# Kernel optimization log

Measured on AMD Instinct MI355X. Metric: run time of the kernel, lower is better.

## Reference

```python
import jax, jax.numpy as jnp
import numpy as np

THRE = 0.5        # communication threshold
ALPHA = 0.8       # S_e / S_c mix in pattern gate
P_BIAS, P_WEIGHT = 0.1, 0.9
DILATE_K = 3
EPS = 1e-6


def warp_affine(src, M, out_hw):
    """torch F.affine_grid + F.grid_sample (bilinear, zeros padding, align_corners=False).
    src: (B,C,Hs,Ws), M: (B,2,3) normalized affine. Returns (B,C,Ho,Wo)."""
    B, C, Hs, Ws = src.shape
    Ho, Wo = out_hw
    xs = 2.0 * (jnp.arange(Wo, dtype=src.dtype) + 0.5) / Wo - 1.0
    ys = 2.0 * (jnp.arange(Ho, dtype=src.dtype) + 0.5) / Ho - 1.0
    gx, gy = jnp.meshgrid(xs, ys)                                   # (Ho,Wo)
    base = jnp.stack([gx, gy, jnp.ones_like(gx)], axis=-1)          # (Ho,Wo,3)
    g = jnp.einsum('bij,hwj->bhwi', M.astype(src.dtype), base)      # (B,Ho,Wo,2) x,y
    px = ((g[..., 0] + 1.0) * Ws - 1.0) * 0.5
    py = ((g[..., 1] + 1.0) * Hs - 1.0) * 0.5
    x0 = jnp.floor(px); y0 = jnp.floor(py)
    wx1 = px - x0; wx0 = 1.0 - wx1
    wy1 = py - y0; wy0 = 1.0 - wy1
    bidx = jnp.arange(B)[:, None, None]
    def samp(yi, xi):
        yi = yi.astype(jnp.int32); xi = xi.astype(jnp.int32)
        valid = (yi >= 0) & (yi < Hs) & (xi >= 0) & (xi < Ws)
        yc = jnp.clip(yi, 0, Hs - 1); xc = jnp.clip(xi, 0, Ws - 1)
        v = src[bidx, :, yc, xc]                                    # (B,Ho,Wo,C)
        return v * valid[..., None].astype(src.dtype)
    out = (samp(y0, x0) * (wy0 * wx0)[..., None]
         + samp(y0, x0 + 1) * (wy0 * wx1)[..., None]
         + samp(y0 + 1, x0) * (wy1 * wx0)[..., None]
         + samp(y0 + 1, x0 + 1) * (wy1 * wx1)[..., None])
    return jnp.transpose(out, (0, 3, 1, 2))


def masked_quantile(xf, mf, q):
    """torch.quantile(x[mask], q) with linear interpolation. xf:(N,HW) float, mf:(N,HW) bool."""
    xs = jnp.sort(jnp.where(mf, xf, jnp.inf), axis=-1)
    cnt = mf.sum(axis=-1)
    pos = q * jnp.maximum(cnt - 1, 0).astype(xf.dtype)
    lo = jnp.floor(pos).astype(jnp.int32)
    hi = jnp.ceil(pos).astype(jnp.int32)
    frac = pos - lo.astype(xf.dtype)
    vlo = jnp.take_along_axis(xs, lo[:, None], axis=-1)[:, 0]
    vhi = jnp.take_along_axis(xs, hi[:, None], axis=-1)[:, 0]
    val = vlo + frac * (vhi - vlo)
    return jnp.where(cnt > 0, val, jnp.zeros_like(val))


def qnorm01(x, mask, ql=0.2, qh=0.8):
    """_qnorm01_masked: per-image masked quantile normalization to [0,1]."""
    N = x.shape[0]
    xf = x.reshape(N, -1)
    mf = mask.reshape(N, -1) > 0
    lo = masked_quantile(xf, mf, ql)[:, None]
    hi = masked_quantile(xf, mf, qh)[:, None]
    y = jnp.clip((xf - lo) / (hi - lo + EPS), 0.0, 1.0) * mf.astype(x.dtype)
    return y.reshape(x.shape)


def pattern_gate(conf_b, feats_b, vis_b):
    """_build_pattern_gate. Returns P (1,1,H,W) on ego plane."""
    visf = (vis_b > 0).astype(feats_b.dtype)
    energy = jnp.mean(feats_b ** 2, axis=1, keepdims=True)          # (N,1,H,W)
    S_e = qnorm01(energy, vis_b) * visf
    S_c_raw = jnp.max(jax.nn.sigmoid(conf_b), axis=1, keepdims=True)  # A>1 branch
    S_c = qnorm01(S_c_raw, vis_b) * visf
    S_mix = ALPHA * S_e + (1.0 - ALPHA) * S_c
    D_e = qnorm01(1.0 - S_e[0:1], vis_b[0:1])
    D_c = qnorm01(1.0 - S_c[0:1], vis_b[0:1])
    D = (0.7 * D_e + 0.3 * D_c) * visf[0:1]
    m0 = vis_b[0:1].reshape(1, -1) > 0
    q20_e = masked_quantile(S_e[0:1].reshape(1, -1), m0, 0.2)[0]
    q20_c = masked_quantile(S_c[0:1].reshape(1, -1), m0, 0.2)[0]
    Ke = (S_e[0:1] <= q20_e) & (vis_b[0:1] > 0)
    Kc = (S_c[0:1] <= q20_c) & (vis_b[0:1] > 0)
    K_empty = (Ke & Kc).astype(feats_b.dtype)
    Sup_nei = jnp.mean(S_mix[1:] * visf[1:], axis=0, keepdims=True)
    P = D * Sup_nei * (1.0 - K_empty)
    return qnorm01(P, vis_b[0:1]) * visf[0:1]


def dilate(mask, k):
    if k <= 1:
        return mask
    return jax.lax.reduce_window(mask, -jnp.inf, jax.lax.max,
                                 (1, 1, k, k), (1, 1, 1, 1), 'SAME')


def owner_for_batch(feats_b, conf_b, vis_b, base_b):
    """_compute_owner_masks_from_comm for one batch group (N agents), eval mode
    (soft_tau=0 -> hard argmax owner), dual_ratio=0, dilate_k=3, supply='cls'."""
    N = feats_b.shape[0]
    visf = (vis_b > 0).astype(feats_b.dtype)
    S_full = jnp.clip(conf_b, 0.0, 1.0).mean(axis=1, keepdims=True) * visf
    P = pattern_gate(conf_b, feats_b, vis_b)                        # (1,1,H,W)
    S_b = S_full * (P_BIAS + P_WEIGHT * P)                          # broadcast over N
    scores = S_b * visf                                             # (N,1,H,W)
    winner = jnp.argmax(scores, axis=0)                             # (1,H,W)
    onehot = (jnp.arange(N)[:, None, None, None] == winner[None]).astype(feats_b.dtype)
    owner = onehot * (base_b > 0).astype(feats_b.dtype)
    return dilate(owner, DILATE_K)


def forward(x, psm_single, record_len, normalized_affine_matrix):
    B, L = normalized_affine_matrix.shape[:2]
    N = L  # uniform record_len assumed (record_len[b] == L for all b)
    sumN, C, H, W = x.shape
    A = psm_single.shape[1]
    # ego-view warp matrices t_matrix[0, :N] per batch, flattened to (B*N,2,3)
    M = normalized_affine_matrix[:, 0].reshape(B * N, 2, 3)
    ones = jnp.ones((B * N, 1, H, W), x.dtype)
    vis = warp_affine(ones, M, (H, W))          # warp masks
    conf = warp_affine(psm_single, M, (H, W))   # warped confidence maps
    wx = warp_affine(x, M, (H, W))              # warped features
    # Communication: where2comm-style threshold on max-sigmoid confidence; ego always ones
    comm_map = jnp.max(jax.nn.sigmoid(conf), axis=1, keepdims=True)
    comm = (comm_map > THRE).astype(x.dtype)
    comm = comm.reshape(B, N, 1, H, W).at[:, 0].set(1.0)            # (B,N,1,H,W)
    owner = jax.vmap(owner_for_batch)(
        wx.reshape(B, N, C, H, W), conf.reshape(B, N, A, H, W),
        vis.reshape(B, N, 1, H, W), comm)                           # (B,N,1,H,W)
    final = comm * owner
    wxm = wx.reshape(B, N, C, H, W) * final
    # effective rate over non-ego agents
    eff = final[:, 1:].sum(axis=(1, 2, 3, 4)) / ((N - 1) * H * W)
    effective_rate = eff.mean()
    x_out = wxm.max(axis=1)                                         # MaxFusion over agents
    return x_out, effective_rate


def setup_inputs():
    key = jax.random.key(0)
    k1, k2, k3 = jax.random.split(key, 3)
    B, N, C, A, H, W = 4, 5, 64, 2, 128, 256
    x = jax.random.normal(k1, (B * N, C, H, W), jnp.float32)
    psm_single = jax.random.normal(k2, (B * N, A, H, W), jnp.float32)
    record_len = jnp.full((B,), N, jnp.int32)
    eye = jnp.tile(jnp.array([[1.0, 0.0, 0.0], [0.0, 1.0, 0.0]], jnp.float32), (B, N, N, 1, 1))
    mats = eye + 0.05 * jax.random.normal(k3, (B, N, N, 2, 3), jnp.float32)
    return {"x": x, "psm_single": psm_single, "record_len": record_len,
            "normalized_affine_matrix": mats}


def reference(x, psm_single, record_len, normalized_affine_matrix):
    return forward(x, psm_single, record_len, normalized_affine_matrix)
```

## Files before the change

kernel.cpp:

```cpp
#include <hip/hip_runtime.h>

#define W_    256
#define H_    128
#define HW_   32768
#define NB    4
#define NA    5
#define NC    64
#define NIMG  20
#define EPS_  1e-6f

struct Taps { int o00,o01,o10,o11; float w00,w01,w10,w11; };

__device__ inline void proj_pt(float M0,float M1,float M2,float M3,float M4,float M5,
                               int h,int w,float&px,float&py){
  float gx = 2.0f*((float)w+0.5f)/(float)W_ - 1.0f;
  float gy = 2.0f*((float)h+0.5f)/(float)H_ - 1.0f;
  float X = M0*gx + M1*gy + M2;
  float Y = M3*gx + M4*gy + M5;
  px = ((X+1.0f)*(float)W_ - 1.0f)*0.5f;
  py = ((Y+1.0f)*(float)H_ - 1.0f)*0.5f;
}

__device__ inline Taps make_taps(const float* __restrict__ M, int h, int w){
  float px,py; proj_pt(M[0],M[1],M[2],M[3],M[4],M[5],h,w,px,py);
  float x0f=floorf(px), y0f=floorf(py);
  float wx1=px-x0f, wx0=1.f-wx1, wy1=py-y0f, wy0=1.f-wy1;
  int x0=(int)x0f, y0=(int)y0f, x1=x0+1, y1=y0+1;
  bool vx0=(x0>=0)&&(x0<W_), vx1=(x1>=0)&&(x1<W_);
  bool vy0=(y0>=0)&&(y0<H_), vy1=(y1>=0)&&(y1<H_);
  int cx0=min(max(x0,0),W_-1), cx1=min(max(x1,0),W_-1);
  int cy0=min(max(y0,0),H_-1), cy1=min(max(y1,0),H_-1);
  Taps t;
  t.o00=cy0*W_+cx0; t.o01=cy0*W_+cx1; t.o10=cy1*W_+cx0; t.o11=cy1*W_+cx1;
  t.w00=(vy0&&vx0)?(wy0*wx0):0.f;
  t.w01=(vy0&&vx1)?(wy0*wx1):0.f;
  t.w10=(vy1&&vx0)?(wy1*wx0):0.f;
  t.w11=(vy1&&vx1)?(wy1*wx1):0.f;
  return t;
}

__device__ inline float clip01(float v){ return fminf(fmaxf(v,0.f),1.f); }
__device__ inline float sigmoidf_(float v){
  if (v>=0.f){ float e=expf(-v); return 1.f/(1.f+e); }
  float e=expf(v); return e/(1.f+e);
}
__device__ inline float quantv(int cnt, float q, float vlo, float vhi){
  if (cnt<=0) return 0.f;
  float pos = q*(float)(cnt-1);
  float frac = pos - floorf(pos);
  return vlo + frac*(vhi-vlo);
}
__device__ inline float ge_f(float t, float lo, float hi){
  return clip01((t-lo)/(hi-lo+EPS_));
}

#define SBAR __builtin_amdgcn_sched_barrier(0)

__global__ void k_init(int* counters){ if (threadIdx.x==0) counters[0] = 0; }

__global__ __launch_bounds__(64) void k_gram(
  const float* __restrict__ x, float* __restrict__ gram)
{
  int lane = threadIdx.x;
  int bx = blockIdx.x;
  int bn = bx >> 7;
  int r  = bx & 127;
  int rn = min(r+1, H_-1);
  int col = lane<<2;
  const float* xb = x + (size_t)bn*NC*HW_;
  float4 aA={0,0,0,0}, aBx={0,0,0,0}, aBy={0,0,0,0}, aBd1={0,0,0,0}, aBd2={0,0,0,0};
  #pragma unroll 4
  for (int c=0;c<NC;++c){
    const float* pc = xb + (size_t)c*HW_;
    float4 a = *reinterpret_cast<const float4*>(pc + r*W_  + col);
    float4 b = *reinterpret_cast<const float4*>(pc + rn*W_ + col);
    float axn = __shfl(a.x, lane+1, 64);
    float bxn = __shfl(b.x, lane+1, 64);
    aA.x  = fmaf(a.x,a.x,aA.x);  aA.y  = fmaf(a.y,a.y,aA.y);
    aA.z  = fmaf(a.z,a.z,aA.z);  aA.w  = fmaf(a.w,a.w,aA.w);
    aBx.x = fmaf(a.x,a.y,aBx.x); aBx.y = fmaf(a.y,a.z,aBx.y);
    aBx.z = fmaf(a.z,a.w,aBx.z); aBx.w = fmaf(a.w,axn,aBx.w);
    aBy.x = fmaf(a.x,b.x,aBy.x); aBy.y = fmaf(a.y,b.y,aBy.y);
    aBy.z = fmaf(a.z,b.z,aBy.z); aBy.w = fmaf(a.w,b.w,aBy.w);
    aBd1.x= fmaf(a.x,b.y,aBd1.x);aBd1.y= fmaf(a.y,b.z,aBd1.y);
    aBd1.z= fmaf(a.z,b.w,aBd1.z);aBd1.w= fmaf(a.w,bxn,aBd1.w);
    aBd2.x= fmaf(a.y,b.x,aBd2.x);aBd2.y= fmaf(a.z,b.y,aBd2.y);
    aBd2.z= fmaf(a.w,b.z,aBd2.z);aBd2.w= fmaf(axn,b.w,aBd2.w);
  }
  float* g0 = gram + (((size_t)bn*HW_ + (size_t)r*W_ + col)<<3);
  float4 lo,hi;
  lo.x=aA.x; lo.y=aBx.x; lo.z=aBy.x; lo.w=aBd1.x; hi.x=aBd2.x; hi.y=0; hi.z=0; hi.w=0;
  *reinterpret_cast<float4*>(g0+ 0)=lo; *reinterpret_cast<float4*>(g0+ 4)=hi;
  lo.x=aA.y; lo.y=aBx.y; lo.z=aBy.y; lo.w=aBd1.y; hi.x=aBd2.y;
  *reinterpret_cast<float4*>(g0+ 8)=lo; *reinterpret_cast<float4*>(g0+12)=hi;
  lo.x=aA.z; lo.y=aBx.z; lo.z=aBy.z; lo.w=aBd1.z; hi.x=aBd2.z;
  *reinterpret_cast<float4*>(g0+16)=lo; *reinterpret_cast<float4*>(g0+20)=hi;
  lo.x=aA.w; lo.y=aBx.w; lo.z=aBy.w; lo.w=aBd1.w; hi.x=aBd2.w;
  *reinterpret_cast<float4*>(g0+24)=lo; *reinterpret_cast<float4*>(g0+28)=hi;
}

__global__ __launch_bounds__(256) void k_warp2(
  const float* __restrict__ psm, const float* __restrict__ nam,
  const float* __restrict__ gram,
  float* __restrict__ vis, float* __restrict__ scraw, float* __restrict__ sfull,
  float* __restrict__ energy)
{
  int w = threadIdx.x, h = blockIdx.x, bn = blockIdx.y;
  int b = bn/NA, n = bn - b*NA;
  const float* M = nam + (size_t)(b*NA*NA + n)*6;
  float px,py; proj_pt(M[0],M[1],M[2],M[3],M[4],M[5],h,w,px,py);
  float x0f=floorf(px), y0f=floorf(py);
  float wx1=px-x0f, wx0=1.f-wx1, wy1=py-y0f, wy0=1.f-wy1;
  int x0=(int)x0f, y0=(int)y0f, x1=x0+1, y1=y0+1;
  bool vx0=(x0>=0)&&(x0<W_), vx1=(x1>=0)&&(x1<W_);
  bool vy0=(y0>=0)&&(y0<H_), vy1=(y1>=0)&&(y1<H_);
  int cx0=min(max(x0,0),W_-1), cx1=min(max(x1,0),W_-1);
  int cy0=min(max(y0,0),H_-1), cy1=min(max(y1,0),H_-1);
  float w00=(vy0&&vx0)?(wy0*wx0):0.f;
  float w01=(vy0&&vx1)?(wy0*wx1):0.f;
  float w10=(vy1&&vx0)?(wy1*wx0):0.f;
  float w11=(vy1&&vx1)?(wy1*wx1):0.f;
  int i00=cy0*W_+cx0, i01=cy0*W_+cx1, i10=cy1*W_+cx0, i11=cy1*W_+cx1;
  float vv = w00+w01+w10+w11;

  const float* p0 = psm + ((size_t)bn*2+0)*HW_;
  const float* p1 = psm + ((size_t)bn*2+1)*HW_;
  float c0 = w00*p0[i00]+w01*p0[i01]+w10*p0[i10]+w11*p0[i11];
  float c1 = w00*p1[i00]+w01*p1[i01]+w10*p1[i10]+w11*p1[i11];

  const float* G = gram + ((size_t)bn*HW_<<3);
  float4 R00 = *reinterpret_cast<const float4*>(G + ((size_t)i00<<3));
  float  D2  = G[((size_t)i00<<3)+4];
  float4 R01 = *reinterpret_cast<const float4*>(G + ((size_t)i01<<3));
  float4 R10 = *reinterpret_cast<const float4*>(G + ((size_t)i10<<3));
  float  A11 = G[(size_t)i11<<3];
  float e = w00*w00*R00.x + w01*w01*R01.x + w10*w10*R10.x + w11*w11*A11
          + 2.0f*( w00*w01*R00.y + w10*w11*R10.y
                 + w00*w10*R00.z + w01*w11*R01.z
                 + w00*w11*R00.w + w01*w10*D2 );

  size_t idx = (size_t)bn*HW_ + (size_t)h*W_ + w;
  vis[idx]=vv;
  scraw[idx]=fmaxf(sigmoidf_(c0), sigmoidf_(c1));
  sfull[idx]=(clip01(c0)+clip01(c1))*0.5f;
  energy[idx]=e*(1.0f/64.0f);
}

#define TWm    32
#define THm    16
#define CAPm   2048
#define TRIPSm 2
#define NBUFm  3
__global__ __launch_bounds__(256) void k_warp_stats_mono(
  const float* __restrict__ x, const float* __restrict__ psm, const float* __restrict__ nam,
  float* __restrict__ vis, float* __restrict__ scraw, float* __restrict__ sfull,
  float* __restrict__ energy)
{
  __shared__ __align__(16) float smem[NBUFm][CAPm];
  int tid = threadIdx.x;
  int tx = blockIdx.x, ty = blockIdx.y, bn = blockIdx.z;
  int b = bn/NA, n = bn - b*NA;
  const float* M = nam + (size_t)(b*NA*NA + n)*6;
  float M0=M[0],M1=M[1],M2=M[2],M3=M[3],M4=M[4],M5=M[5];
  int tw0 = tx*TWm, th0 = ty*THm;
  int r  = tid>>4;
  int cb = (tid&15)<<1;
  int h  = th0 + r;
  int w0 = tw0 + cb;
  float pxa,pya,pxb,pyb,pxc,pyc,pxd,pyd;
  proj_pt(M0,M1,M2,M3,M4,M5, th0,       tw0,       pxa,pya);
  proj_pt(M0,M1,M2,M3,M4,M5, th0,       tw0+TWm-1, pxb,pyb);
  proj_pt(M0,M1,M2,M3,M4,M5, th0+THm-1, tw0,       pxc,pyc);
  proj_pt(M0,M1,M2,M3,M4,M5, th0+THm-1, tw0+TWm-1, pxd,pyd);
  float pxmin=fminf(fminf(pxa,pxb),fminf(pxc,pxd));
  float pxmax=fmaxf(fmaxf(pxa,pxb),fmaxf(pxc,pxd));
  float pymin=fminf(fminf(pya,pyb),fminf(pyc,pyd));
  float pymax=fmaxf(fmaxf(pya,pyb),fmaxf(pyc,pyd));
  int xs = min(max((int)floorf(pxmin)-1, 0), W_-1);
  int xe = min(max((int)floorf(pxmax)+2, 0), W_-1);
  int ys = min(max((int)floorf(pymin)-1, 0), H_-1);
  int ye = min(max((int)floorf(pymax)+2, 0), H_-1);
  int xs4 = xs & ~3;
  int bwid = xe - xs4 + 1, bh = ye - ys + 1;
  int nck = (bwid+3)>>2;
  int bwp = nck<<2;
  int E2 = bh*bwp;
  bool ok = (E2 <= CAPm);
  float vvv[2], w00_[2],w01_[2],w10_[2],w11_[2];
  int   gx0[2],gx1[2],gy0c[2],gy1c[2];
  int   rx0[2]; bool vx0f[2];
  #pragma unroll
  for (int k=0;k<2;++k){
    float px,py; proj_pt(M0,M1,M2,M3,M4,M5, h, w0+k, px,py);
    float x0f=floorf(px), y0f=floorf(py);
    float wx1=px-x0f, wx0=1.f-wx1, wy1=py-y0f, wy0=1.f-wy1;
    int x0=(int)x0f, y0=(int)y0f, x1=x0+1, y1=y0+1;
    bool vx0=(x0>=0)&&(x0<W_), vx1=(x1>=0)&&(x1<W_);
    bool vy0=(y0>=0)&&(y0<H_), vy1=(y1>=0)&&(y1<H_);
    float w00=(vy0&&vx0)?(wy0*wx0):0.f;
    float w01=(vy0&&vx1)?(wy0*wx1):0.f;
    float w10=(vy1&&vx0)?(wy1*wx0):0.f;
    float w11=(vy1&&vx1)?(wy1*wx1):0.f;
    w00_[k]=w00; w01_[k]=w01; w10_[k]=w10; w11_[k]=w11;
    vvv[k]=w00+w01+w10+w11;
    gx0[k]=min(max(x0,0),W_-1); gx1[k]=min(max(x1,0),W_-1);
    gy0c[k]=min(max(y0,0),H_-1); gy1c[k]=min(max(y1,0),H_-1);
    rx0[k]=x0; vx0f[k]=vx0;
  }
  size_t idx = (size_t)bn*HW_ + (size_t)h*W_ + w0;
  float acc[2] = {0.f,0.f};
  int srcoff[TRIPSm]; int ldsbase = (tid>>6)<<6;
  const float* xb0 = x + (size_t)bn*NC*HW_ + (size_t)ys*W_ + xs4;
  if (ok){
    int totq = bh*nck;
    unsigned magic = (unsigned)((0x100000000ULL + (unsigned)nck - 1) / (unsigned)nck);
    int colcap = (W_-4) - xs4;
    #pragma unroll
    for (int k=0;k<TRIPSm;++k){
      int qq = min(tid + (k<<8), totq-1);
      int row = (int)__umulhi((unsigned)qq, magic);
      int col = (qq - row*nck)<<2;
      srcoff[k] = row*W_ + min(col, colcap);
    }
  }
  auto issue = [&](int ch, int bsel){
    const float* src = xb0 + (size_t)ch*HW_;
    #pragma unroll
    for (int k=0;k<TRIPSm;++k){
      __builtin_amdgcn_global_load_lds(
        (const __attribute__((address_space(1))) void*)(src + srcoff[k]),
        (__attribute__((address_space(3))) void*)&smem[bsel][(ldsbase + (k<<8))<<2],
        16, 0, 0);
    }
  };
  if (ok){ issue(0,0); issue(1,1); }
  {
    const float* p0 = psm + ((size_t)bn*2+0)*HW_;
    const float* p1 = psm + ((size_t)bn*2+1)*HW_;
    #pragma unroll
    for (int k=0;k<2;++k){
      int o00=gy0c[k]*W_+gx0[k], o01=gy0c[k]*W_+gx1[k];
      int o10=gy1c[k]*W_+gx0[k], o11=gy1c[k]*W_+gx1[k];
      float c0 = w00_[k]*p0[o00]+w01_[k]*p0[o01]+w10_[k]*p0[o10]+w11_[k]*p0[o11];
      float c1 = w00_[k]*p1[o00]+w01_[k]*p1[o01]+w10_[k]*p1[o10]+w11_[k]*p1[o11];
      vis[idx+k]   = vvv[k];
      scraw[idx+k] = fmaxf(sigmoidf_(c0), sigmoidf_(c1));
      sfull[idx+k] = (clip01(c0)+clip01(c1))*0.5f;
    }
  }
  if (ok){
    int a0[2],a1[2]; float e0[2],e1[2],f0[2],f1[2];
    #pragma unroll
    for (int k=0;k<2;++k){
      int bc = min(max(rx0[k]-xs4,0), bwp-1);
      a0[k] = (gy0c[k]-ys)*bwp + bc;
      a1[k] = (gy1c[k]-ys)*bwp + bc;
      bool v0 = vx0f[k];
      e0[k] = v0 ? w00_[k] : w01_[k];
      e1[k] = v0 ? w01_[k] : 0.f;
      f0[k] = v0 ? w10_[k] : w11_[k];
      f1[k] = v0 ? w11_[k] : 0.f;
    }
    #pragma unroll 1
    for (int c=0;c<NC;++c){
      asm volatile("s_waitcnt vmcnt(2)" ::: "memory"); SBAR;
      __builtin_amdgcn_s_barrier(); SBAR;
      {
        int nc2 = c+2 < NC ? c+2 : NC-1;
        issue(nc2, (c+2)%NBUFm);
      }
      const float* B = smem[c%NBUFm];
      #pragma unroll
      for (int k=0;k<2;++k){
        float r00=B[a0[k]], r01=B[a0[k]+1];
        float r10=B[a1[k]], r11=B[a1[k]+1];
        float v = e0[k]*r00 + e1[k]*r01 + f0[k]*r10 + f1[k]*r11;
        acc[k] += v*v;
      }
    }
    asm volatile("s_waitcnt vmcnt(0)" ::: "memory");
  } else {
    const float* xb = x + (size_t)bn*NC*HW_;
    int go00[2],go01[2],go10[2],go11[2];
    #pragma unroll
    for (int k=0;k<2;++k){
      go00[k]=gy0c[k]*W_+gx0[k]; go01[k]=gy0c[k]*W_+gx1[k];
      go10[k]=gy1c[k]*W_+gx0[k]; go11[k]=gy1c[k]*W_+gx1[k];
    }
    for (int c=0;c<NC;++c){
      const float* pc = xb + (size_t)c*HW_;
      #pragma unroll
      for (int k=0;k<2;++k){
        float v = w00_[k]*pc[go00[k]] + w01_[k]*pc[go01[k]]
                + w10_[k]*pc[go10[k]] + w11_[k]*pc[go11[k]];
        acc[k] += v*v;
      }
    }
  }
  #pragma unroll
  for (int k=0;k<2;++k) energy[idx+k] = acc[k]*(1.0f/64.0f);
}

#define OS_T 1024
__global__ __launch_bounds__(1024) void k_select(
    const float* __restrict__ energy, const float* __restrict__ scraw,
    const float* __restrict__ ppre, const float* __restrict__ vis,
    float* __restrict__ statsE, float* __restrict__ statsC, float* __restrict__ statsP,
    int mode)
{
  __shared__ int hist[16*256];
  __shared__ int cum[256];
  __shared__ unsigned s_pre;
  __shared__ int s_rk;
  __shared__ int s_cnt;
  int tid = threadIdx.x;
  int t = blockIdx.x;

  const float* d; const float* m; float* stats; int img, r;
  if (mode==0){
    bool isC = (t>=96); int tt = isC ? t-96 : t;
    if (tt<80){ img=tt>>2; r=tt&3; } else { int j=tt-80; img=(j>>2)*NA; r=4+(j&3); }
    d = (isC?scraw:energy) + (size_t)img*HW_;
    m = vis + (size_t)img*HW_;
    stats = isC?statsC:statsE;
  } else {
    img = t>>2; r = t&3;
    d = ppre + (size_t)img*HW_;
    m = vis + (size_t)(img*NA)*HW_;
    stats = statsP;
  }

  if (tid==0) s_cnt = 0;
  __syncthreads();

  unsigned key[32];
  int cc = 0;
  #pragma unroll
  for (int k=0;k<32;++k){
    int i = tid + (k<<10);
    unsigned u = __float_as_uint(d[i]);
    unsigned kk = (u & 0x80000000u) ? ~u : (u|0x80000000u);
    bool valid = (m[i] > 0.f);
    key[k] = valid ? kk : 0xFFFFFFFFu;
    cc += valid ? 1 : 0;
  }
  #pragma unroll
  for (int off=32;off;off>>=1) cc += __shfl_down(cc,off);
  if ((tid&63)==0) atomicAdd(&s_cnt, cc);
  __syncthreads();
  int cnt = s_cnt;
  int cm1 = cnt>0 ? cnt-1 : 0;
  float p2 = 0.2f*(float)cm1, p8 = 0.8f*(float)cm1;
  int l2=(int)floorf(p2), h2=(int)ceilf(p2), l8=(int)floorf(p8), h8=(int)ceilf(p8);
  int rank;
  switch(r){
    case 0: rank=l2; break;      case 1: rank=h2; break;
    case 2: rank=l8; break;      case 3: rank=h8; break;
    case 4: rank=cm1-l2; break;  case 5: rank=cm1-h2; break;
    case 6: rank=cm1-l8; break;  default: rank=cm1-h8; break;
  }
  if (tid==0){ s_pre=0u; s_rk=rank; }
  int slice = tid & 15;
  #pragma unroll
  for (int round=0; round<4; ++round){
    const int shift = 24 - 8*round;
    for (int i=tid;i<16*256;i+=OS_T) hist[i]=0;
    __syncthreads();
    unsigned pre = s_pre;
    if (round==0){
      #pragma unroll
      for (int k=0;k<32;++k)
        atomicAdd(&hist[slice*256 + (key[k]>>24)], 1);
    } else {
      #pragma unroll
      for (int k=0;k<32;++k)
        if ((key[k]>>(shift+8)) == pre)
          atomicAdd(&hist[slice*256 + ((key[k]>>shift)&255u)], 1);
    }
    __syncthreads();
    if (tid<256){
      int tt2=0;
      #pragma unroll
      for (int s=0;s<16;++s) tt2 += hist[s*256+tid];
      cum[tid]=tt2;
    }
    __syncthreads();
    if (tid<64){
      int c0=cum[4*tid+0],c1=cum[4*tid+1],c2=cum[4*tid+2],c3=cum[4*tid+3];
      int i0=c0, i1=i0+c1, i2=i1+c2, i3=i2+c3;
      int tot=i3, scan=tot;
      #pragma unroll
      for (int off=1;off<64;off<<=1){ int v=__shfl_up(scan,off); if (tid>=off) scan+=v; }
      int base = scan-tot;
      int rk = s_rk; unsigned pr = s_pre;
      int b0=base, b1=base+i0, b2=base+i1, b3=base+i2, e3=base+i3;
      if      (rk>=b0 && rk<b1){ s_pre=(pr<<8)|(unsigned)(4*tid+0); s_rk=rk-b0; }
      else if (rk>=b1 && rk<b2){ s_pre=(pr<<8)|(unsigned)(4*tid+1); s_rk=rk-b1; }
      else if (rk>=b2 && rk<b3){ s_pre=(pr<<8)|(unsigned)(4*tid+2); s_rk=rk-b2; }
      else if (rk>=b3 && rk<e3){ s_pre=(pr<<8)|(unsigned)(4*tid+3); s_rk=rk-b3; }
    }
    __syncthreads();
  }
  if (tid==0){
    unsigned k = s_pre;
    unsigned u = (k & 0x80000000u) ? (k & 0x7FFFFFFFu) : ~k;
    stats[img*16 + 1 + r] = __uint_as_float(u);
    if (r==0) stats[img*16] = (float)cnt;
  }
}

__global__ void k_params(const float* __restrict__ statsE, const float* __restrict__ statsC,
                         float* __restrict__ params){
  int b = threadIdx.x;
  if (b>=NB) return;
  float* pr = params + b*32;
  for (int n=0;n<NA;++n){
    const float* sE = statsE + (size_t)(b*NA+n)*16;
    const float* sC = statsC + (size_t)(b*NA+n)*16;
    int cE=(int)sE[0], cC=(int)sC[0];
    pr[n]    = quantv(cE,0.2f,sE[1],sE[2]);
    pr[5+n]  = quantv(cE,0.8f,sE[3],sE[4]);
    pr[10+n] = quantv(cC,0.2f,sC[1],sC[2]);
    pr[15+n] = quantv(cC,0.8f,sC[3],sC[4]);
  }
  const float* sE0 = statsE + (size_t)(b*NA)*16;
  const float* sC0 = statsC + (size_t)(b*NA)*16;
  float loe=pr[0], hie=pr[5], loc=pr[10], hic=pr[15];
  float de_lo=0.f,de_hi=0.f,ke=0.f, dc_lo=0.f,dc_hi=0.f,kc=0.f;
  int c0=(int)sE0[0];
  if (c0>0){
    int cm1=c0-1;
    float pos2=0.2f*(float)cm1, pos8=0.8f*(float)cm1;
    float f2=pos2-floorf(pos2), f8=pos8-floorf(pos8);
    float a,bb;
    a=1.f-ge_f(sE0[5],loe,hie); bb=1.f-ge_f(sE0[6],loe,hie); de_lo=a+f2*(bb-a);
    a=1.f-ge_f(sE0[7],loe,hie); bb=1.f-ge_f(sE0[8],loe,hie); de_hi=a+f8*(bb-a);
    a=ge_f(sE0[1],loe,hie);     bb=ge_f(sE0[2],loe,hie);     ke  =a+f2*(bb-a);
  }
  int c0c=(int)sC0[0];
  if (c0c>0){
    int cm1=c0c-1;
    float pos2=0.2f*(float)cm1, pos8=0.8f*(float)cm1;
    float f2=pos2-floorf(pos2), f8=pos8-floorf(pos8);
    float a,bb;
    a=1.f-ge_f(sC0[5],loc,hic); bb=1.f-ge_f(sC0[6],loc,hic); dc_lo=a+f2*(bb-a);
    a=1.f-ge_f(sC0[7],loc,hic); bb=1.f-ge_f(sC0[8],loc,hic); dc_hi=a+f8*(bb-a);
    a=ge_f(sC0[1],loc,hic);     bb=ge_f(sC0[2],loc,hic);     kc  =a+f2*(bb-a);
  }
  pr[20]=de_lo; pr[21]=de_hi; pr[22]=dc_lo; pr[23]=dc_hi; pr[24]=ke; pr[25]=kc;
}

__global__ __launch_bounds__(256) void k_ppre(
  const float* __restrict__ vis, const float* __restrict__ scraw,
  const float* __restrict__ energy, const float* __restrict__ params,
  float* __restrict__ ppre)
{
  int w=threadIdx.x, h=blockIdx.x, b=blockIdx.y;
  int p=h*W_+w;
  const float* pr = params + b*32;
  size_t base = (size_t)b*NA*HW_ + p;
  float se[NA], sc[NA], vf[NA];
  #pragma unroll
  for (int n=0;n<NA;++n){
    float vv = vis[base + (size_t)n*HW_];
    float f = (vv>0.f)?1.f:0.f; vf[n]=f;
    se[n] = clip01((energy[base+(size_t)n*HW_]-pr[n])/(pr[5+n]-pr[n]+EPS_))*f;
    sc[n] = clip01((scraw[base+(size_t)n*HW_]-pr[10+n])/(pr[15+n]-pr[10+n]+EPS_))*f;
  }
  float sup = 0.f;
  #pragma unroll
  for (int n=1;n<NA;++n) sup += (0.8f*se[n]+0.2f*sc[n])*vf[n];
  sup *= 0.25f;
  float de = clip01(((1.f-se[0])-pr[20])/(pr[21]-pr[20]+EPS_))*vf[0];
  float dc = clip01(((1.f-sc[0])-pr[22])/(pr[23]-pr[22]+EPS_))*vf[0];
  float D  = (0.7f*de + 0.3f*dc)*vf[0];
  bool ke = (se[0] <= pr[24]) && (vf[0]>0.f);
  bool kc = (sc[0] <= pr[25]) && (vf[0]>0.f);
  float kem = (ke&&kc)?1.f:0.f;
  ppre[(size_t)b*HW_+p] = D*sup*(1.f-kem);
}

__global__ __launch_bounds__(256) void k_owner(
  const float* __restrict__ vis, const float* __restrict__ scraw,
  const float* __restrict__ sfull, const float* __restrict__ ppre,
  const float* __restrict__ statsP, int* __restrict__ omask)
{
  int w=threadIdx.x,h=blockIdx.x,b=blockIdx.y;
  int p=h*W_+w;
  const float* sP = statsP + b*16;
  int cntP=(int)sP[0];
  float plo = quantv(cntP,0.2f,sP[1],sP[2]);
  float phi = quantv(cntP,0.8f,sP[3],sP[4]);
  size_t base=(size_t)b*NA*HW_+p;
  float vf0 = (vis[base]>0.f)?1.f:0.f;
  float Pf = clip01((ppre[(size_t)b*HW_+p]-plo)/(phi-plo+EPS_))*vf0;
  float gate = 0.1f + 0.9f*Pf;
  int winner=0; float best=-1.f;
  int cbits=0;
  #pragma unroll
  for (int n=0;n<NA;++n){
    float vv = vis[base+(size_t)n*HW_];
    float f=(vv>0.f)?1.f:0.f;
    float s = ((sfull[base+(size_t)n*HW_]*f)*gate)*f;
    if (s>best){best=s;winner=n;}
    bool cm = (n==0) || (scraw[base+(size_t)n*HW_] > 0.5f);
    if (cm) cbits |= 1<<n;
  }
  int ob = ((cbits>>winner)&1) ? (1<<winner) : 0;
  omask[(size_t)b*HW_+p] = ob | (cbits<<8);
}

__global__ __launch_bounds__(256) void k_final(
  const int* __restrict__ omask, int* __restrict__ fmask, int* __restrict__ counter)
{
  int w=threadIdx.x,h=blockIdx.x,b=blockIdx.y;
  int p=h*W_+w;
  const int* om = omask + (size_t)b*HW_;
  int ow=0;
  #pragma unroll
  for (int dy=-1;dy<=1;++dy){
    int y=h+dy; if (y<0||y>=H_) continue;
    #pragma unroll
    for (int dx=-1;dx<=1;++dx){
      int x=w+dx; if (x<0||x>=W_) continue;
      ow |= om[y*W_+x];
    }
  }
  int cbits=(om[p]>>8)&31;
  int fin = ow & cbits & 31;
  fmask[(size_t)b*HW_+p]=fin;
  int cn = __popc(fin & 30);
  for (int off=32;off;off>>=1) cn += __shfl_down(cn,off);
  if ((threadIdx.x&63)==0) atomicAdd(counter, cn);
}

__global__ __launch_bounds__(256, 2) void k_out(
  const float* __restrict__ x, const float* __restrict__ nam,
  const int* __restrict__ fmask, const int* __restrict__ counter,
  float* __restrict__ out, int out_size)
{
  int w=threadIdx.x, h=blockIdx.x, b=blockIdx.y;
  int p=h*W_+w;
  int fin = fmask[(size_t)b*HW_+p] & 31;
  float init = (__popc(fin)<NA) ? 0.f : -__builtin_inff();
  Taps tp[NA];
  #pragma unroll
  for (int n=0;n<NA;++n) tp[n] = make_taps(nam + (size_t)(b*NA*NA+n)*6, h, w);
  #pragma unroll 1
  for (int cb=0; cb<NC/16; ++cb){
    float m[16];
    #pragma unroll
    for (int c=0;c<16;++c) m[c]=init;
    #pragma unroll
    for (int n=0;n<NA;++n){
      if (!((fin>>n)&1)) continue;
      const float* pc = x + ((size_t)(b*NA+n)*NC + cb*16)*HW_;
      float a00[16],a01[16],a10[16],a11[16];
      #pragma unroll
      for (int c=0;c<16;++c){
        a00[c]=pc[tp[n].o00]; a01[c]=pc[tp[n].o01]; a10[c]=pc[tp[n].o10]; a11[c]=pc[tp[n].o11];
        pc += HW_;
      }
      #pragma unroll
      for (int c=0;c<16;++c){
        float v = tp[n].w00*a00[c] + tp[n].w01*a01[c] + tp[n].w10*a10[c] + tp[n].w11*a11[c];
        m[c] = fmaxf(m[c], v);
      }
    }
    #pragma unroll
    for (int c=0;c<16;++c)
      out[(((size_t)b*NC + cb*16 + c)*H_+h)*W_+w] = m[c];
  }
  if (b==0 && h==0 && w==0)
    out[out_size-1] = (float)(*counter) * (1.0f/524288.0f);
}

extern "C" void kernel_launch(void* const* d_in, const int* in_sizes, int n_in,
                              void* d_out, int out_size, void* d_ws, size_t ws_size,
                              hipStream_t stream) {
  (void)in_sizes; (void)n_in;
  const float* x   = (const float*)d_in[0];
  const float* psm = (const float*)d_in[1];
  const float* nam = (const float*)d_in[3];
  float* out = (float*)d_out;

  float* ws     = (float*)d_ws;
  float* vis    = ws;
  float* scraw  = vis    + (size_t)NIMG*HW_;
  float* sfull  = scraw  + (size_t)NIMG*HW_;
  float* energy = sfull  + (size_t)NIMG*HW_;
  float* ppre   = energy + (size_t)NIMG*HW_;
  float* statsE = ppre   + (size_t)NB*HW_;
  float* statsC = statsE + NIMG*16;
  float* statsP = statsC + NIMG*16;
  float* params = statsP + NB*16;
  int*   omask  = (int*)(params + NB*32);
  int*   fmask  = omask + (size_t)NB*HW_;
  int*   counter= fmask + (size_t)NB*HW_;
  float* gram   = (float*)(counter + 64);
  size_t need = (size_t)((gram + ((size_t)NIMG*HW_<<3)) - ws) * sizeof(float);

  hipLaunchKernelGGL(k_init, dim3(1), dim3(64), 0, stream, counter);
  if (ws_size >= need){
    hipLaunchKernelGGL(k_gram, dim3(NIMG*H_), dim3(64), 0, stream, x, gram);
    hipLaunchKernelGGL(k_warp2, dim3(H_,NIMG), dim3(W_), 0, stream,
                       psm, nam, gram, vis, scraw, sfull, energy);
  } else {
    hipLaunchKernelGGL(k_warp_stats_mono, dim3(W_/TWm, H_/THm, NIMG), dim3(256), 0, stream,
                       x, psm, nam, vis, scraw, sfull, energy);
  }
  hipLaunchKernelGGL(k_select, dim3(192), dim3(OS_T), 0, stream,
                     energy, scraw, ppre, vis, statsE, statsC, statsP, 0);
  hipLaunchKernelGGL(k_params, dim3(1), dim3(64), 0, stream, statsE, statsC, params);
  hipLaunchKernelGGL(k_ppre, dim3(H_,NB), dim3(W_), 0, stream,
                     vis, scraw, energy, params, ppre);
  hipLaunchKernelGGL(k_select, dim3(16), dim3(OS_T), 0, stream,
                     energy, scraw, ppre, vis, statsE, statsC, statsP, 1);
  hipLaunchKernelGGL(k_owner, dim3(H_,NB), dim3(W_), 0, stream,
                     vis, scraw, sfull, ppre, statsP, omask);
  hipLaunchKernelGGL(k_final, dim3(H_,NB), dim3(W_), 0, stream, omask, fmask, counter);
  hipLaunchKernelGGL(k_out, dim3(H_,NB), dim3(W_), 0, stream,
                     x, nam, fmask, counter, out, out_size);
}
```

Before: 227.0 us.

## Vectorize bilinear tap gathers with aligned float4 loads and swizzle gram blocks

```diff
diff --git a/kernel.cpp b/kernel.cpp
--- a/kernel.cpp
+++ b/kernel.cpp
@@ -53,6 +53,9 @@
 __device__ inline float ge_f(float t, float lo, float hi){
   return clip01((t-lo)/(hi-lo+EPS_));
 }
+__device__ inline float sel4(float4 q, int i){
+  return i==0 ? q.x : (i==1 ? q.y : (i==2 ? q.z : q.w));
+}
 
 #define SBAR __builtin_amdgcn_sched_barrier(0)
 
@@ -63,8 +66,9 @@
 {
   int lane = threadIdx.x;
   int bx = blockIdx.x;
-  int bn = bx >> 7;
-  int r  = bx & 127;
+  int lin = (bx&7)*(NIMG*H_/8) + (bx>>3);
+  int bn = lin >> 7;
+  int r  = lin & 127;
   int rn = min(r+1, H_-1);
   int col = lane<<2;
   const float* xb = x + (size_t)bn*NC*HW_;
@@ -543,33 +547,62 @@
   int p=h*W_+w;
   int fin = fmask[(size_t)b*HW_+p] & 31;
   float init = (__popc(fin)<NA) ? 0.f : -__builtin_inff();
-  Taps tp[NA];
-  #pragma unroll
-  for (int n=0;n<NA;++n) tp[n] = make_taps(nam + (size_t)(b*NA*NA+n)*6, h, w);
+  int oq0[NA], oq1[NA], li0[NA], li1[NA], os0[NA], os1[NA];
+  bool sep[NA];
+  float wa[NA],wb[NA],wc[NA],wd[NA];
+  #pragma unroll
+  for (int n=0;n<NA;++n){
+    Taps t = make_taps(nam + (size_t)(b*NA*NA+n)*6, h, w);
+    int cx0 = t.o00 & (W_-1);
+    int cx1 = t.o01 & (W_-1);
+    int r0  = t.o00 - cx0;
+    int r1  = t.o10 - cx0;
+    int q   = cx0 & ~3;
+    oq0[n] = r0 + q; oq1[n] = r1 + q;
+    li0[n] = cx0 & 3;
+    int l1 = cx1 - q;
+    sep[n] = (l1 > 3);
+    li1[n] = sep[n] ? 0 : l1;
+    os0[n] = r0 + cx1; os1[n] = r1 + cx1;
+    wa[n]=t.w00; wb[n]=t.w01; wc[n]=t.w10; wd[n]=t.w11;
+  }
   #pragma unroll 1
-  for (int cb=0; cb<NC/16; ++cb){
-    float m[16];
-    #pragma unroll
-    for (int c=0;c<16;++c) m[c]=init;
+  for (int cb=0; cb<NC/8; ++cb){
+    float m[8];
+    #pragma unroll
+    for (int c=0;c<8;++c) m[c]=init;
     #pragma unroll
     for (int n=0;n<NA;++n){
       if (!((fin>>n)&1)) continue;
-      const float* pc = x + ((size_t)(b*NA+n)*NC + cb*16)*HW_;
-      float a00[16],a01[16],a10[16],a11[16];
-      #pragma unroll
-      for (int c=0;c<16;++c){
-        a00[c]=pc[tp[n].o00]; a01[c]=pc[tp[n].o01]; a10[c]=pc[tp[n].o10]; a11[c]=pc[tp[n].o11];
-        pc += HW_;
+      const float* pc = x + ((size_t)(b*NA+n)*NC + cb*8)*HW_;
+      float4 Q0[8], Q1[8];
+      float  S0[8]={0,0,0,0,0,0,0,0}, S1[8]={0,0,0,0,0,0,0,0};
+      {
+        const float* pp = pc;
+        #pragma unroll
+        for (int c=0;c<8;++c){
+          Q0[c] = *reinterpret_cast<const float4*>(pp + oq0[n]);
+          Q1[c] = *reinterpret_cast<const float4*>(pp + oq1[n]);
+          pp += HW_;
+        }
+      }
+      if (sep[n]){
+        const float* ps = pc;
+        #pragma unroll
+        for (int c=0;c<8;++c){ S0[c]=ps[os0[n]]; S1[c]=ps[os1[n]]; ps += HW_; }
       }
       #pragma unroll
-      for (int c=0;c<16;++c){
-        float v = tp[n].w00*a00[c] + tp[n].w01*a01[c] + tp[n].w10*a10[c] + tp[n].w11*a11[c];
-        m[c] = fmaxf(m[c], v);
+      for (int c=0;c<8;++c){
+        float v00 = sel4(Q0[c], li0[n]);
+        float v10 = sel4(Q1[c], li0[n]);
+        float v01 = sep[n] ? S0[c] : sel4(Q0[c], li1[n]);
+        float v11 = sep[n] ? S1[c] : sel4(Q1[c], li1[n]);
+        m[c] = fmaxf(m[c], wa[n]*v00 + wb[n]*v01 + wc[n]*v10 + wd[n]*v11);
       }
     }
     #pragma unroll
-    for (int c=0;c<16;++c)
-      out[(((size_t)b*NC + cb*16 + c)*H_+h)*W_+w] = m[c];
+    for (int c=0;c<8;++c)
+      out[(((size_t)b*NC + cb*8 + c)*H_+h)*W_+w] = m[c];
   }
   if (b==0 && h==0 && w==0)
     out[out_size-1] = (float)(*counter) * (1.0f/524288.0f);
```

Result: slower. 259.9 us (+14.5%).
